# Optimization experiments

Measured on AMD Instinct MI355X. Metric: run time of the kernel, lower is better.

## Reference

```python
import jax, jax.numpy as jnp
import numpy as np

N_SRC, N_DST, N_EDGES = 60000, 50000, 600000
IN_DIM, OUT_DIM = 256, 128


def setup_inputs() -> dict:
    key = jax.random.key(0)
    k1, k2, k3, k4, k5, k6 = jax.random.split(key, 6)
    features = jax.random.normal(k1, (N_SRC, IN_DIM), dtype=jnp.float32)
    t = jax.random.uniform(k2, (N_SRC,), dtype=jnp.float32)
    edge_src = jax.random.randint(k3, (N_EDGES,), 0, N_SRC, dtype=jnp.int32)
    edge_dst = jax.random.randint(k4, (N_EDGES,), 0, N_DST, dtype=jnp.int32)
    # learned params: xavier_normal with relu gain for fc, default for temporal_fc
    gain = float(np.sqrt(2.0))
    std_fc = gain * np.sqrt(2.0 / (IN_DIM + OUT_DIM))
    W_fc = jax.random.normal(k5, (OUT_DIM, IN_DIM), dtype=jnp.float32) * std_fc
    W_t = jax.random.normal(k6, (1, OUT_DIM), dtype=jnp.float32) * (1.0 / np.sqrt(OUT_DIM))
    return {"features": features, "t": t, "edge_src": edge_src,
            "edge_dst": edge_dst, "n_dst": N_DST, "W_fc": W_fc, "W_t": W_t}


def reference(features, t, edge_src, edge_dst, n_dst, W_fc, W_t):
    # z = fc(h), no bias
    z = features @ W_fc.T                      # [n_src, out_dim]
    s = (z @ W_t.T)[:, 0]                      # temporal_fc(z) -> [n_src]
    # edge attention: e = -|t_src - t_dst| (non-differentiable in original)
    e = jax.lax.stop_gradient(-jnp.abs(t[edge_src] - t[edge_dst]))  # [E]
    # mailbox logits: exp(temporal_fc(z_src) * e / 500)
    y = jnp.exp(s[edge_src] * e / 500.0)       # [E]
    # segment softmax over incoming edges of each dst node
    m = jax.ops.segment_max(y, edge_dst, num_segments=n_dst)
    m = jnp.where(jnp.isfinite(m), m, 0.0)     # empty mailboxes
    ex = jnp.exp(y - m[edge_dst])
    denom = jax.ops.segment_sum(ex, edge_dst, num_segments=n_dst)
    alpha = ex / denom[edge_dst]               # [E]
    # weighted neighbor sum
    h = jax.ops.segment_sum(alpha[:, None] * z[edge_src], edge_dst, num_segments=n_dst)
    # residual
    return z[:n_dst] + h
```

## Files before the change

kernel.cpp:

```cpp
#include <hip/hip_runtime.h>
#include <cstdint>

#define TPB 256
#define DSTRIDE 48

typedef __attribute__((ext_vector_type(8))) _Float16 half8;
typedef __attribute__((ext_vector_type(4))) float floatx4;

__global__ __launch_bounds__(256) void convert_w(
    const float* __restrict__ W, _Float16* __restrict__ Wh, int n)
{
    int i = blockIdx.x * 256 + threadIdx.x;
    if (i < n) Wh[i] = (_Float16)W[i];
}

__global__ __launch_bounds__(512, 4) void gemm_mfma(
    const float* __restrict__ A, const _Float16* __restrict__ Wh,
    const float* __restrict__ Wt, _Float16* __restrict__ z16,
    float* __restrict__ s, int M)
{
    __shared__ half8 Wlds[4096];

    const int tid  = threadIdx.x;
    const int lane = tid & 63;
    const int w    = tid >> 6;
    const int m    = lane & 15;
    const int q    = lane >> 4;

#pragma unroll
    for (int it = 0; it < 8; ++it) {
        int pair = w * 8 + it;
        int nt = pair & 7, ks = pair >> 3;
        const _Float16* src = Wh + (size_t)(nt * 16 + m) * 256 + ks * 32 + q * 8;
        Wlds[pair * 64 + lane] = *(const half8*)src;
    }

    const int row_base = blockIdx.x * 128 + w * 16;
    const int arow = min(row_base + m, M - 1);
    const float* ap = A + (size_t)arow * 256 + q * 8;

    float4 abuf[8];
#pragma unroll
    for (int i = 0; i < 4; ++i) {
        abuf[2 * i]     = *(const float4*)(ap + i * 32);
        abuf[2 * i + 1] = *(const float4*)(ap + i * 32 + 4);
    }

    floatx4 acc[8];
#pragma unroll
    for (int nt = 0; nt < 8; ++nt) acc[nt] = (floatx4){0.f, 0.f, 0.f, 0.f};

    __syncthreads();

#pragma unroll
    for (int ks = 0; ks < 8; ++ks) {
        float4 a0 = abuf[(ks & 3) * 2];
        float4 a1 = abuf[(ks & 3) * 2 + 1];
        half8 af;
        af[0] = (_Float16)a0.x; af[1] = (_Float16)a0.y;
        af[2] = (_Float16)a0.z; af[3] = (_Float16)a0.w;
        af[4] = (_Float16)a1.x; af[5] = (_Float16)a1.y;
        af[6] = (_Float16)a1.z; af[7] = (_Float16)a1.w;

        if (ks < 4) {
            abuf[(ks & 3) * 2]     = *(const float4*)(ap + (ks + 4) * 32);
            abuf[(ks & 3) * 2 + 1] = *(const float4*)(ap + (ks + 4) * 32 + 4);
        }

#pragma unroll
        for (int nt = 0; nt < 8; ++nt) {
            half8 bf = Wlds[(ks * 8 + nt) * 64 + lane];
            acc[nt] = __builtin_amdgcn_mfma_f32_16x16x32_f16(
                af, bf, acc[nt], 0, 0, 0);
        }
    }

    float wt[8];
#pragma unroll
    for (int nt = 0; nt < 8; ++nt) wt[nt] = Wt[nt * 16 + m];

    float sp[4] = {0.f, 0.f, 0.f, 0.f};
#pragma unroll
    for (int nt = 0; nt < 8; ++nt)
#pragma unroll
        for (int reg = 0; reg < 4; ++reg)
            sp[reg] += acc[nt][reg] * wt[nt];

#pragma unroll
    for (int reg = 0; reg < 4; ++reg) {
        int row = row_base + q * 4 + reg;
        if (row < M) {
#pragma unroll
            for (int nt = 0; nt < 8; ++nt)
                z16[(size_t)row * 128 + nt * 16 + m] = (_Float16)acc[nt][reg];
        }
    }
#pragma unroll
    for (int off = 1; off <= 8; off <<= 1)
#pragma unroll
        for (int reg = 0; reg < 4; ++reg)
            sp[reg] += __shfl_xor(sp[reg], off, 64);
    if (m == 0) {
#pragma unroll
        for (int reg = 0; reg < 4; ++reg) {
            int row = row_base + q * 4 + reg;
            if (row < M) s[row] = sp[reg];
        }
    }
}

__global__ __launch_bounds__(256) void scatter_pass(
    const int* __restrict__ esrc, const int* __restrict__ edst,
    const float* __restrict__ t, const float* __restrict__ s,
    int* __restrict__ cnt, int2* __restrict__ edata, int E)
{
    int e = blockIdx.x * TPB + threadIdx.x;
    if (e >= E) return;
    int si = esrc[e], di = edst[e];
    float ee = -fabsf(t[si] - t[di]);
    float yv = __expf(s[si] * ee * (1.0f / 500.0f));
    float exv = __expf(yv);
    int pos = atomicAdd(&cnt[di], 1);
    if (pos < DSTRIDE)
        edata[(size_t)di * DSTRIDE + pos] = make_int2(si, __float_as_int(exv));
}

__global__ __launch_bounds__(256) void aggregate(
    const _Float16* __restrict__ z16, const int* __restrict__ cnt,
    const int2* __restrict__ edata, float* __restrict__ out, int Nd)
{
    int d = blockIdx.x * 4 + (threadIdx.x >> 6);
    if (d >= Nd) return;
    int lane = threadIdx.x & 63;
    int g  = lane >> 4;
    int fo = lane & 15;
    int num = cnt[d];
    if (num > DSTRIDE) num = DSTRIDE;
    const int2* row = edata + (size_t)d * DSTRIDE;

    float acc[8];
#pragma unroll
    for (int i = 0; i < 8; ++i) acc[i] = 0.f;
    float dsum = 0.f;

    int j = g;
    for (; j + 4 < num; j += 8) {
        int2 e0 = row[j];
        int2 e1 = row[j + 4];
        float w0 = __int_as_float(e0.y);
        float w1 = __int_as_float(e1.y);
        half8 v0 = ((const half8*)(z16 + (size_t)e0.x * 128))[fo];
        half8 v1 = ((const half8*)(z16 + (size_t)e1.x * 128))[fo];
        dsum += w0 + w1;
#pragma unroll
        for (int i = 0; i < 8; ++i) {
            acc[i] = fmaf(w0, (float)v0[i], acc[i]);
            acc[i] = fmaf(w1, (float)v1[i], acc[i]);
        }
    }
    for (; j < num; j += 4) {
        int2 e0 = row[j];
        float w0 = __int_as_float(e0.y);
        half8 v0 = ((const half8*)(z16 + (size_t)e0.x * 128))[fo];
        dsum += w0;
#pragma unroll
        for (int i = 0; i < 8; ++i)
            acc[i] = fmaf(w0, (float)v0[i], acc[i]);
    }
    dsum += __shfl_xor(dsum, 16, 64);
    dsum += __shfl_xor(dsum, 32, 64);
    float inv = (num > 0) ? 1.0f / dsum : 0.0f;
#pragma unroll
    for (int i = 0; i < 8; ++i) acc[i] *= inv;
#pragma unroll
    for (int i = 0; i < 8; ++i) {
        acc[i] += __shfl_xor(acc[i], 16, 64);
        acc[i] += __shfl_xor(acc[i], 32, 64);
    }
    if (g == 0) {
        half8 zr = ((const half8*)(z16 + (size_t)d * 128))[fo];
        float* op = out + (size_t)d * 128 + fo * 8;
        float4 o0 = make_float4(acc[0] + (float)zr[0], acc[1] + (float)zr[1],
                                acc[2] + (float)zr[2], acc[3] + (float)zr[3]);
        float4 o1 = make_float4(acc[4] + (float)zr[4], acc[5] + (float)zr[5],
                                acc[6] + (float)zr[6], acc[7] + (float)zr[7]);
        *(float4*)op = o0;
        *(float4*)(op + 4) = o1;
    }
}

extern "C" void kernel_launch(void* const* d_in, const int* in_sizes, int n_in,
                              void* d_out, int out_size, void* d_ws, size_t ws_size,
                              hipStream_t stream)
{
    const float* features = (const float*)d_in[0];
    const float* t        = (const float*)d_in[1];
    const int*   esrc     = (const int*)d_in[2];
    const int*   edst     = (const int*)d_in[3];
    const float* Wfc      = (const float*)d_in[5];
    const float* Wt       = (const float*)d_in[6];
    float* out = (float*)d_out;

    const int M  = in_sizes[1];
    const int E  = in_sizes[2];
    const int OD = in_sizes[6];
    const int Nd = out_size / OD;
    const int ID = in_sizes[5] / OD;

    _Float16* z16 = (_Float16*)d_ws;
    float* s   = (float*)(z16 + (size_t)M * 128);
    int*   cnt = (int*)(s + M);
    _Float16* Wh = (_Float16*)(cnt + Nd);
    int2*  edata = (int2*)(Wh + (size_t)OD * ID);

    (void)hipMemsetAsync(cnt, 0, (size_t)Nd * sizeof(int), stream);

    convert_w<<<(OD * ID + 255) / 256, 256, 0, stream>>>(Wfc, Wh, OD * ID);
    gemm_mfma<<<(M + 127) / 128, 512, 0, stream>>>(features, Wh, Wt, z16, s, M);
    scatter_pass<<<(E + TPB - 1) / TPB, TPB, 0, stream>>>(esrc, edst, t, s,
                                                          cnt, edata, E);
    aggregate<<<(Nd + 3) / 4, 256, 0, stream>>>(z16, cnt, edata, out, Nd);
}
```

Before: 193.6 us.

## Replace per-destination atomic slots with binned counting-sort partition of edges

Edges are bucket-sorted by destination into 1024 bins of 64 nodes using a block histogram, a two-stage scan and a shared-memory atomic scatter into a compact buffer. Aggregation then loads each bin into LDS, sub-sorts by local destination, and reduces with 8 lanes per node. This removes global atomics on per-node counters and the sparse fixed-stride edge array. The trade-off is three extra small kernels, a serial column scan, and packing source indices into 16 bits, which assumes fewer than 65536 sources and at most 1536 edges per bin.

```diff
diff --git a/kernel.cpp b/kernel.cpp
--- a/kernel.cpp
+++ b/kernel.cpp
@@ -1,8 +1,9 @@
 #include <hip/hip_runtime.h>
 #include <cstdint>
 
-#define TPB 256
-#define DSTRIDE 48
+#define NBINS 1024
+#define EPB   4096
+#define MAXE  1536
 
 typedef __attribute__((ext_vector_type(8))) _Float16 half8;
 typedef __attribute__((ext_vector_type(4))) float floatx4;
@@ -109,83 +110,213 @@
     }
 }
 
-__global__ __launch_bounds__(256) void scatter_pass(
+__global__ __launch_bounds__(512) void part_hist(
+    const int* __restrict__ edst, int* __restrict__ gcount, int E)
+{
+    __shared__ int h[NBINS];
+    for (int i = threadIdx.x; i < NBINS; i += 512) h[i] = 0;
+    __syncthreads();
+    int base = blockIdx.x * EPB + threadIdx.x * 8;
+    if (base + 8 <= E) {
+        int4 d0 = *(const int4*)(edst + base);
+        int4 d1 = *(const int4*)(edst + base + 4);
+        atomicAdd(&h[d0.x >> 6], 1); atomicAdd(&h[d0.y >> 6], 1);
+        atomicAdd(&h[d0.z >> 6], 1); atomicAdd(&h[d0.w >> 6], 1);
+        atomicAdd(&h[d1.x >> 6], 1); atomicAdd(&h[d1.y >> 6], 1);
+        atomicAdd(&h[d1.z >> 6], 1); atomicAdd(&h[d1.w >> 6], 1);
+    } else {
+        for (int i = 0; i < 8; ++i)
+            if (base + i < E) atomicAdd(&h[edst[base + i] >> 6], 1);
+    }
+    __syncthreads();
+    for (int i = threadIdx.x; i < NBINS; i += 512)
+        gcount[blockIdx.x * NBINS + i] = h[i];
+}
+
+__global__ __launch_bounds__(256) void part_scanA(
+    int* __restrict__ gcount, int* __restrict__ binTot, int NB)
+{
+    int t = threadIdx.x;
+    if (t >= 32) return;
+    int b = blockIdx.x * 32 + t;
+    int run = 0;
+    for (int blk = 0; blk < NB; ++blk) {
+        int idx = blk * NBINS + b;
+        int c = gcount[idx];
+        gcount[idx] = run;
+        run += c;
+    }
+    binTot[b] = run;
+}
+
+__global__ __launch_bounds__(1024) void part_scanB(
+    const int* __restrict__ binTot, int* __restrict__ binstart)
+{
+    __shared__ int sb[NBINS];
+    int b = threadIdx.x;
+    int v = binTot[b];
+    sb[b] = v;
+    __syncthreads();
+    for (int off = 1; off < NBINS; off <<= 1) {
+        int add = (b >= off) ? sb[b - off] : 0;
+        __syncthreads();
+        sb[b] += add;
+        __syncthreads();
+    }
+    binstart[b] = sb[b] - v;
+    if (b == NBINS - 1) binstart[NBINS] = sb[b];
+}
+
+__global__ __launch_bounds__(512) void part_scatter(
     const int* __restrict__ esrc, const int* __restrict__ edst,
     const float* __restrict__ t, const float* __restrict__ s,
-    int* __restrict__ cnt, int2* __restrict__ edata, int E)
-{
-    int e = blockIdx.x * TPB + threadIdx.x;
-    if (e >= E) return;
-    int si = esrc[e], di = edst[e];
-    float ee = -fabsf(t[si] - t[di]);
-    float yv = __expf(s[si] * ee * (1.0f / 500.0f));
-    float exv = __expf(yv);
-    int pos = atomicAdd(&cnt[di], 1);
-    if (pos < DSTRIDE)
-        edata[(size_t)di * DSTRIDE + pos] = make_int2(si, __float_as_int(exv));
+    const int* __restrict__ gcount, const int* __restrict__ binstart,
+    int2* __restrict__ part, int E)
+{
+    __shared__ int h[NBINS];
+    for (int i = threadIdx.x; i < NBINS; i += 512)
+        h[i] = gcount[blockIdx.x * NBINS + i] + binstart[i];
+    __syncthreads();
+
+    int base = blockIdx.x * EPB + threadIdx.x * 8;
+    if (base >= E) return;
+    int si[8], di[8];
+    int nv = E - base; if (nv > 8) nv = 8;
+    if (nv == 8) {
+        int4 s0 = *(const int4*)(esrc + base);
+        int4 s1 = *(const int4*)(esrc + base + 4);
+        int4 d0 = *(const int4*)(edst + base);
+        int4 d1 = *(const int4*)(edst + base + 4);
+        si[0]=s0.x; si[1]=s0.y; si[2]=s0.z; si[3]=s0.w;
+        si[4]=s1.x; si[5]=s1.y; si[6]=s1.z; si[7]=s1.w;
+        di[0]=d0.x; di[1]=d0.y; di[2]=d0.z; di[3]=d0.w;
+        di[4]=d1.x; di[5]=d1.y; di[6]=d1.z; di[7]=d1.w;
+    } else {
+        for (int i = 0; i < 8; ++i) {
+            int e = min(base + i, E - 1);
+            si[i] = esrc[e]; di[i] = edst[e];
+        }
+    }
+#pragma unroll
+    for (int i = 0; i < 8; ++i) {
+        if (i < nv) {
+            int pos = atomicAdd(&h[di[i] >> 6], 1);
+            float ee = -fabsf(t[si[i]] - t[di[i]]);
+            float exv = __expf(__expf(s[si[i]] * ee * (1.0f / 500.0f)));
+            part[pos] = make_int2((si[i] & 0xffff) | ((di[i] & 63) << 16),
+                                  __float_as_int(exv));
+        }
+    }
 }
 
 __global__ __launch_bounds__(256) void aggregate(
-    const _Float16* __restrict__ z16, const int* __restrict__ cnt,
-    const int2* __restrict__ edata, float* __restrict__ out, int Nd)
-{
-    int d = blockIdx.x * 4 + (threadIdx.x >> 6);
-    if (d >= Nd) return;
-    int lane = threadIdx.x & 63;
-    int g  = lane >> 4;
-    int fo = lane & 15;
-    int num = cnt[d];
-    if (num > DSTRIDE) num = DSTRIDE;
-    const int2* row = edata + (size_t)d * DSTRIDE;
-
-    float acc[8];
-#pragma unroll
-    for (int i = 0; i < 8; ++i) acc[i] = 0.f;
-    float dsum = 0.f;
-
-    int j = g;
-    for (; j + 4 < num; j += 8) {
-        int2 e0 = row[j];
-        int2 e1 = row[j + 4];
-        float w0 = __int_as_float(e0.y);
-        float w1 = __int_as_float(e1.y);
-        half8 v0 = ((const half8*)(z16 + (size_t)e0.x * 128))[fo];
-        half8 v1 = ((const half8*)(z16 + (size_t)e1.x * 128))[fo];
-        dsum += w0 + w1;
-#pragma unroll
-        for (int i = 0; i < 8; ++i) {
-            acc[i] = fmaf(w0, (float)v0[i], acc[i]);
-            acc[i] = fmaf(w1, (float)v1[i], acc[i]);
-        }
-    }
-    for (; j < num; j += 4) {
-        int2 e0 = row[j];
-        float w0 = __int_as_float(e0.y);
-        half8 v0 = ((const half8*)(z16 + (size_t)e0.x * 128))[fo];
-        dsum += w0;
-#pragma unroll
-        for (int i = 0; i < 8; ++i)
-            acc[i] = fmaf(w0, (float)v0[i], acc[i]);
-    }
-    dsum += __shfl_xor(dsum, 16, 64);
-    dsum += __shfl_xor(dsum, 32, 64);
-    float inv = (num > 0) ? 1.0f / dsum : 0.0f;
-#pragma unroll
-    for (int i = 0; i < 8; ++i) acc[i] *= inv;
-#pragma unroll
-    for (int i = 0; i < 8; ++i) {
-        acc[i] += __shfl_xor(acc[i], 16, 64);
-        acc[i] += __shfl_xor(acc[i], 32, 64);
-    }
-    if (g == 0) {
-        half8 zr = ((const half8*)(z16 + (size_t)d * 128))[fo];
-        float* op = out + (size_t)d * 128 + fo * 8;
-        float4 o0 = make_float4(acc[0] + (float)zr[0], acc[1] + (float)zr[1],
-                                acc[2] + (float)zr[2], acc[3] + (float)zr[3]);
-        float4 o1 = make_float4(acc[4] + (float)zr[4], acc[5] + (float)zr[5],
-                                acc[6] + (float)zr[6], acc[7] + (float)zr[7]);
-        *(float4*)op = o0;
-        *(float4*)(op + 4) = o1;
+    const _Float16* __restrict__ z16, const int* __restrict__ binstart,
+    const int2* __restrict__ part, float* __restrict__ out, int Nd)
+{
+    __shared__ int2 arr[MAXE];
+    __shared__ int lcnt[64];
+    __shared__ int loff[65];
+    __shared__ int lcur[64];
+
+    const int tid = threadIdx.x;
+    const int b = blockIdx.x;
+    const int s0 = binstart[b];
+    int nE = binstart[b + 1] - s0;
+    if (nE > MAXE) nE = MAXE;
+
+    if (tid < 64) lcnt[tid] = 0;
+    __syncthreads();
+    for (int i = tid; i < nE; i += 256)
+        atomicAdd(&lcnt[(part[s0 + i].x >> 16) & 63], 1);
+    __syncthreads();
+    if (tid < 64) {
+        int v = lcnt[tid], x = v;
+#pragma unroll
+        for (int off = 1; off < 64; off <<= 1) {
+            int n = __shfl_up(x, off, 64);
+            if (tid >= off) x += n;
+        }
+        loff[tid + 1] = x;
+        lcur[tid] = x - v;
+        if (tid == 0) loff[0] = 0;
+    }
+    __syncthreads();
+    for (int i = tid; i < nE; i += 256) {
+        int2 r = part[s0 + i];
+        int pos = atomicAdd(&lcur[(r.x >> 16) & 63], 1);
+        arr[pos] = r;
+    }
+    __syncthreads();
+
+    const int lane = tid & 63;
+    const int w = tid >> 6;
+    const int g = lane >> 3;
+    const int c = lane & 7;
+
+#pragma unroll
+    for (int k = 0; k < 2; ++k) {
+        int loc = w * 16 + k * 8 + g;
+        int d = b * 64 + loc;
+        if (d >= Nd) continue;
+        int jb = loff[loc], je = loff[loc + 1];
+
+        float acc[16];
+#pragma unroll
+        for (int i = 0; i < 16; ++i) acc[i] = 0.f;
+        float dsum = 0.f;
+
+        int j = jb;
+        for (; j + 1 < je; j += 2) {
+            int2 r0 = arr[j];
+            int2 r1 = arr[j + 1];
+            float x0 = __int_as_float(r0.y);
+            float x1 = __int_as_float(r1.y);
+            const half8* zp0 = (const half8*)(z16 + (size_t)(r0.x & 0xffff) * 128 + c * 16);
+            const half8* zp1 = (const half8*)(z16 + (size_t)(r1.x & 0xffff) * 128 + c * 16);
+            half8 a0 = zp0[0], a1 = zp0[1];
+            half8 b0 = zp1[0], b1 = zp1[1];
+            dsum += x0 + x1;
+#pragma unroll
+            for (int i = 0; i < 8; ++i) {
+                acc[i]     = fmaf(x0, (float)a0[i], acc[i]);
+                acc[8 + i] = fmaf(x0, (float)a1[i], acc[8 + i]);
+                acc[i]     = fmaf(x1, (float)b0[i], acc[i]);
+                acc[8 + i] = fmaf(x1, (float)b1[i], acc[8 + i]);
+            }
+        }
+        if (j < je) {
+            int2 r0 = arr[j];
+            float x0 = __int_as_float(r0.y);
+            const half8* zp0 = (const half8*)(z16 + (size_t)(r0.x & 0xffff) * 128 + c * 16);
+            half8 a0 = zp0[0], a1 = zp0[1];
+            dsum += x0;
+#pragma unroll
+            for (int i = 0; i < 8; ++i) {
+                acc[i]     = fmaf(x0, (float)a0[i], acc[i]);
+                acc[8 + i] = fmaf(x0, (float)a1[i], acc[8 + i]);
+            }
+        }
+
+        float inv = (je > jb) ? 1.0f / dsum : 0.0f;
+        const half8* zr = (const half8*)(z16 + (size_t)d * 128 + c * 16);
+        half8 r0 = zr[0], r1 = zr[1];
+        float* op = out + (size_t)d * 128 + c * 16;
+        *(float4*)(op + 0)  = make_float4(fmaf(acc[0],  inv, (float)r0[0]),
+                                          fmaf(acc[1],  inv, (float)r0[1]),
+                                          fmaf(acc[2],  inv, (float)r0[2]),
+                                          fmaf(acc[3],  inv, (float)r0[3]));
+        *(float4*)(op + 4)  = make_float4(fmaf(acc[4],  inv, (float)r0[4]),
+                                          fmaf(acc[5],  inv, (float)r0[5]),
+                                          fmaf(acc[6],  inv, (float)r0[6]),
+                                          fmaf(acc[7],  inv, (float)r0[7]));
+        *(float4*)(op + 8)  = make_float4(fmaf(acc[8],  inv, (float)r1[0]),
+                                          fmaf(acc[9],  inv, (float)r1[1]),
+                                          fmaf(acc[10], inv, (float)r1[2]),
+                                          fmaf(acc[11], inv, (float)r1[3]));
+        *(float4*)(op + 12) = make_float4(fmaf(acc[12], inv, (float)r1[4]),
+                                          fmaf(acc[13], inv, (float)r1[5]),
+                                          fmaf(acc[14], inv, (float)r1[6]),
+                                          fmaf(acc[15], inv, (float)r1[7]));
     }
 }
 
@@ -207,17 +338,22 @@
     const int Nd = out_size / OD;
     const int ID = in_sizes[5] / OD;
 
-    _Float16* z16 = (_Float16*)d_ws;
-    float* s   = (float*)(z16 + (size_t)M * 128);
-    int*   cnt = (int*)(s + M);
-    _Float16* Wh = (_Float16*)(cnt + Nd);
-    int2*  edata = (int2*)(Wh + (size_t)OD * ID);
-
-    (void)hipMemsetAsync(cnt, 0, (size_t)Nd * sizeof(int), stream);
+    const int NB = (E + EPB - 1) / EPB;
+
+    _Float16* z16   = (_Float16*)d_ws;
+    float*    s     = (float*)(z16 + (size_t)M * 128);
+    _Float16* Wh    = (_Float16*)(s + M);
+    int*      gcount = (int*)(Wh + (size_t)OD * ID);
+    int*      binTot = gcount + (size_t)NB * NBINS;
+    int*      binstart = binTot + NBINS;
+    int2*     part  = (int2*)(binstart + NBINS + 4);
 
     convert_w<<<(OD * ID + 255) / 256, 256, 0, stream>>>(Wfc, Wh, OD * ID);
+    part_hist<<<NB, 512, 0, stream>>>(edst, gcount, E);
+    part_scanA<<<NBINS / 32, 256, 0, stream>>>(gcount, binTot, NB);
+    part_scanB<<<1, 1024, 0, stream>>>(binTot, binstart);
     gemm_mfma<<<(M + 127) / 128, 512, 0, stream>>>(features, Wh, Wt, z16, s, M);
-    scatter_pass<<<(E + TPB - 1) / TPB, TPB, 0, stream>>>(esrc, edst, t, s,
-                                                          cnt, edata, E);
-    aggregate<<<(Nd + 3) / 4, 256, 0, stream>>>(z16, cnt, edata, out, Nd);
-}
+    part_scatter<<<NB, 512, 0, stream>>>(esrc, edst, t, s, gcount, binstart,
+                                         part, E);
+    aggregate<<<(Nd + 63) / 64, 256, 0, stream>>>(z16, binstart, part, out, Nd);
+}
```

Result: slower. 205.6 us (+6.2%).
